# Performance work log

Hardware: AMD Instinct MI355X
Metric: run time of the kernel (lower is better)

Reference implementation:

```python
import jax, jax.numpy as jnp
import numpy as np

N = 50000      # nodes
DEG = 16       # incoming edges per node
E = N * DEG    # edges
F = 256        # nfeat
H = 8          # heads
DH = 32        # nhid // nheads
ALPHA = 0.2    # LeakyReLU negative slope


def setup_inputs() -> dict:
    key = jax.random.key(0)
    ks = jax.random.split(key, 6)
    h = jax.random.normal(ks[0], (N, F), jnp.float32)
    # xavier_uniform-like scale for W (gain 1.414)
    lim_w = 1.414 * np.sqrt(6.0 / (F + DH))
    W = jax.random.uniform(ks[1], (H, F, DH), jnp.float32, -lim_w, lim_w)
    bW = jnp.zeros((H, DH), jnp.float32)
    lim_a = 1.414 * np.sqrt(6.0 / (2 * DH + 1))
    a_src = jax.random.uniform(ks[2], (H, DH), jnp.float32, -lim_a, lim_a)
    a_dst = jax.random.uniform(ks[3], (H, DH), jnp.float32, -lim_a, lim_a)
    a_bias = jnp.zeros((H,), jnp.float32)
    src = jax.random.randint(ks[4], (E,), 0, N, dtype=jnp.int32)
    # every node gets exactly DEG incoming edges (ensures non-empty mailbox)
    dst = jnp.repeat(jnp.arange(N, dtype=jnp.int32), DEG)
    return {"h": h, "W": W, "bW": bW, "a_src": a_src, "a_dst": a_dst,
            "a_bias": a_bias, "src": src, "dst": dst}


def reference(h, W, bW, a_src, a_dst, a_bias, src, dst):
    # per-head projection: Wh[n,h,d]
    Wh = jnp.einsum('nf,hfd->nhd', h, W) + bW
    # decomposed attention linear: a([Wh_src, Wh_dst]) = s1[src] + s2[dst] + b
    s1 = jnp.einsum('nhd,hd->nh', Wh, a_src)   # [N,H]
    s2 = jnp.einsum('nhd,hd->nh', Wh, a_dst)   # [N,H]
    e = jax.nn.leaky_relu(s1[src] + s2[dst] + a_bias, ALPHA)  # [E,H]
    # segment softmax over incoming edges per destination node
    m = jax.ops.segment_max(e, dst, num_segments=N)           # [N,H]
    ex = jnp.exp(e - m[dst])
    denom = jax.ops.segment_sum(ex, dst, num_segments=N)      # [N,H]
    attn = ex / denom[dst]                                    # [E,H]
    # weighted scatter-sum aggregation of source features
    hp = jax.ops.segment_sum(attn[:, :, None] * Wh[src], dst, num_segments=N)  # [N,H,DH]
    # concat heads (matches torch.cat over head outputs)
    return hp.reshape(N, H * DH)
```

## Files before the change

kernel.cpp:

```cpp
#include <hip/hip_runtime.h>

#define NNODES 50000
#define FEAT 256
#define NH 8
#define DHEAD 32
#define DEG 16
#define CDIM 256

typedef __attribute__((ext_vector_type(4))) float floatx4;
typedef __attribute__((ext_vector_type(8))) short shortx8;

__device__ __forceinline__ unsigned short f2bf(float f) {
  union { float f; unsigned u; } v; v.f = f;
  unsigned r = v.u + 0x7fffu + ((v.u >> 16) & 1u);
  return (unsigned short)(r >> 16);
}
__device__ __forceinline__ float bf2f(unsigned short b) {
  union { unsigned u; float f; } v; v.u = ((unsigned)b) << 16;
  return v.f;
}

__global__ __launch_bounds__(256) void convert_wt(
    const float* __restrict__ W, unsigned short* __restrict__ Wt2) {
  int t = blockIdx.x * 256 + threadIdx.x;
#pragma unroll
  for (int p = 0; p < 4; ++p) {
    int idx = t * 4 + p;
    int jj = idx & 7;
    int l = (idx >> 3) & 63;
    int kt = (idx >> 9) & 7;
    int cgrp = idx >> 12;
    int c = cgrp * 16 + (l & 15);
    int f = kt * 32 + ((l >> 4) << 3) + jj;
    Wt2[idx] = f2bf(W[(size_t)(c >> 5) * (FEAT * DHEAD) + (size_t)f * DHEAD + (c & 31)]);
  }
}

__global__ __launch_bounds__(256) void gemm_fused(
    const float* __restrict__ h, const unsigned short* __restrict__ Wt2,
    const float* __restrict__ bW, const float* __restrict__ a_src,
    const float* __restrict__ a_dst, const float* __restrict__ a_bias,
    unsigned short* __restrict__ Whb, float* __restrict__ s1g,
    float* __restrict__ s2g) {
  __shared__ unsigned short As2[8 * 4 * 64 * 8];
  const int tid = threadIdx.x;
  const int w = tid >> 6, lane = tid & 63;
  const int mrow = lane & 15, quad = lane >> 4;
  const int row0 = blockIdx.x * 64;

  {
    int grow = row0 + w * 16 + mrow;
    if (grow > NNODES - 1) grow = NNODES - 1;
    const float* hp = h + (size_t)grow * FEAT + quad * 8;
#pragma unroll
    for (int kt = 0; kt < 8; ++kt) {
      float4 v0 = *(const float4*)(hp + kt * 32);
      float4 v1 = *(const float4*)(hp + kt * 32 + 4);
      shortx8 a8;
      a8[0] = (short)f2bf(v0.x); a8[1] = (short)f2bf(v0.y);
      a8[2] = (short)f2bf(v0.z); a8[3] = (short)f2bf(v0.w);
      a8[4] = (short)f2bf(v1.x); a8[5] = (short)f2bf(v1.y);
      a8[6] = (short)f2bf(v1.z); a8[7] = (short)f2bf(v1.w);
      *(shortx8*)&As2[((kt * 4 + w) * 64 + lane) * 8] = a8;
    }
  }
  __syncthreads();

  floatx4 acc[4][4] = {};
#pragma unroll
  for (int kt = 0; kt < 8; ++kt) {
    shortx8 af[4], bfr[4];
#pragma unroll
    for (int ni = 0; ni < 4; ++ni) {
      int cgrp = w * 4 + ni;
      bfr[ni] = *(const shortx8*)&Wt2[((size_t)(cgrp * 8 + kt) * 64 + lane) * 8];
    }
#pragma unroll
    for (int mi = 0; mi < 4; ++mi)
      af[mi] = *(const shortx8*)&As2[((kt * 4 + mi) * 64 + lane) * 8];
#pragma unroll
    for (int mi = 0; mi < 4; ++mi)
#pragma unroll
      for (int ni = 0; ni < 4; ++ni)
        acc[mi][ni] = __builtin_amdgcn_mfma_f32_16x16x32_bf16(
            af[mi], bfr[ni], acc[mi][ni], 0, 0, 0);
  }

  float aw_s[4], aw_d[4], bias[4];
#pragma unroll
  for (int ni = 0; ni < 4; ++ni) {
    int col = w * 64 + ni * 16 + mrow;
    aw_s[ni] = a_src[col];
    aw_d[ni] = a_dst[col];
    bias[ni] = bW[col];
  }
  float ab0 = a_bias[w * 2], ab1 = a_bias[w * 2 + 1];
#pragma unroll
  for (int mi = 0; mi < 4; ++mi) {
#pragma unroll
    for (int ni = 0; ni < 4; ++ni) {
      int col = w * 64 + ni * 16 + mrow;
#pragma unroll
      for (int r = 0; r < 4; ++r) {
        int row = row0 + mi * 16 + quad * 4 + r;
        float val = acc[mi][ni][r] + bias[ni];
        acc[mi][ni][r] = val;
        if (row < NNODES) Whb[(size_t)row * CDIM + col] = f2bf(val);
      }
    }
#pragma unroll
    for (int r = 0; r < 4; ++r) {
      float s1h0 = acc[mi][0][r] * aw_s[0] + acc[mi][1][r] * aw_s[1];
      float s1h1 = acc[mi][2][r] * aw_s[2] + acc[mi][3][r] * aw_s[3];
      float s2h0 = acc[mi][0][r] * aw_d[0] + acc[mi][1][r] * aw_d[1];
      float s2h1 = acc[mi][2][r] * aw_d[2] + acc[mi][3][r] * aw_d[3];
#pragma unroll
      for (int off = 1; off < 16; off <<= 1) {
        s1h0 += __shfl_xor(s1h0, off, 64);
        s1h1 += __shfl_xor(s1h1, off, 64);
        s2h0 += __shfl_xor(s2h0, off, 64);
        s2h1 += __shfl_xor(s2h1, off, 64);
      }
      if (mrow == 0) {
        int row = row0 + mi * 16 + quad * 4 + r;
        if (row < NNODES) {
          float2 s1v; s1v.x = s1h0; s1v.y = s1h1;
          float2 s2v; s2v.x = s2h0 + ab0; s2v.y = s2h1 + ab1;
          *(float2*)&s1g[(size_t)row * NH + w * 2] = s1v;
          *(float2*)&s2g[(size_t)row * NH + w * 2] = s2v;
        }
      }
    }
  }
}

__global__ __launch_bounds__(256) void aggregate(
    const unsigned short* __restrict__ Whb, const float* __restrict__ s1g,
    const float* __restrict__ s2g, const int* __restrict__ src,
    float* __restrict__ out) {
  __shared__ int srcs_s[4][DEG];
  __shared__ float sc_s[4][DEG * NH];
  int wave = threadIdx.x >> 6, lane = threadIdx.x & 63;
  int n = blockIdx.x * 4 + wave;
  if (lane < DEG) srcs_s[wave][lane] = src[(size_t)n * DEG + lane];
  __syncthreads();

  ushort4 vrows[DEG];
#pragma unroll
  for (int e = 0; e < DEG; ++e)
    vrows[e] = *(const ushort4*)&Whb[(size_t)srcs_s[wave][e] * CDIM + lane * 4];

  int hh7 = lane & 7;
  float s2v = s2g[(size_t)n * NH + hh7];
#pragma unroll
  for (int p = 0; p < 2; ++p) {
    int i = lane + p * 64;
    int e = i >> 3;
    int s = srcs_s[wave][e];
    float sc = s1g[(size_t)s * NH + hh7] + s2v;
    sc_s[wave][i] = sc > 0.f ? sc : 0.2f * sc;
  }
  __syncthreads();
  if (lane < 8) {
    float m = -1e30f;
#pragma unroll
    for (int e = 0; e < DEG; ++e) m = fmaxf(m, sc_s[wave][e * 8 + lane]);
    float sum = 0.f;
#pragma unroll
    for (int e = 0; e < DEG; ++e) {
      float ex = __expf(sc_s[wave][e * 8 + lane] - m);
      sc_s[wave][e * 8 + lane] = ex;
      sum += ex;
    }
    float inv = 1.f / sum;
#pragma unroll
    for (int e = 0; e < DEG; ++e) sc_s[wave][e * 8 + lane] *= inv;
  }
  __syncthreads();

  int hh = lane >> 3;
  floatx4 acc = {0.f, 0.f, 0.f, 0.f};
#pragma unroll
  for (int e = 0; e < DEG; ++e) {
    float wgt = sc_s[wave][e * 8 + hh];
    ushort4 v = vrows[e];
    acc.x += wgt * bf2f(v.x);
    acc.y += wgt * bf2f(v.y);
    acc.z += wgt * bf2f(v.z);
    acc.w += wgt * bf2f(v.w);
  }
  __builtin_nontemporal_store(acc, (floatx4*)&out[(size_t)n * CDIM + lane * 4]);
}

extern "C" void kernel_launch(void* const* d_in, const int* in_sizes, int n_in,
                              void* d_out, int out_size, void* d_ws, size_t ws_size,
                              hipStream_t stream) {
  const float* h = (const float*)d_in[0];
  const float* W = (const float*)d_in[1];
  const float* bW = (const float*)d_in[2];
  const float* a_src = (const float*)d_in[3];
  const float* a_dst = (const float*)d_in[4];
  const float* a_bias = (const float*)d_in[5];
  const int* src = (const int*)d_in[6];
  float* out = (float*)d_out;

  unsigned short* Whb = (unsigned short*)d_ws;
  unsigned short* Wt2 = Whb + (size_t)NNODES * CDIM;
  float* s1g = (float*)(Wt2 + CDIM * FEAT);
  float* s2g = s1g + (size_t)NNODES * NH;

  convert_wt<<<64, 256, 0, stream>>>(W, Wt2);
  gemm_fused<<<(NNODES + 63) / 64, 256, 0, stream>>>(h, Wt2, bW, a_src, a_dst,
                                                     a_bias, Whb, s1g, s2g);
  aggregate<<<NNODES / 4, 256, 0, stream>>>(Whb, s1g, s2g, src, out);
}
```

Measured before the change: 198.3 us.

## Rewrite aggregate kernel with wave shuffles instead of shared memory and barriers

Replaces the shared-memory staging of source indices and attention scores, and the three block barriers, with wave-level shuffles. The segment softmax is now computed cooperatively by all 64 lanes through xor-shuffle reductions, instead of only 8 lanes looping serially over 16 edges. Feature gathers use 16-byte loads, with each half-wave covering half of the edges; the two partial sums are combined by a cross-half shuffle before a select-and-store. This is meant to cut barrier and LDS latency and serial softmax work, at the cost of extra shuffle instructions and higher register pressure.

```diff
diff --git a/kernel.cpp b/kernel.cpp
--- a/kernel.cpp
+++ b/kernel.cpp
@@ -9,6 +9,7 @@
 
 typedef __attribute__((ext_vector_type(4))) float floatx4;
 typedef __attribute__((ext_vector_type(8))) short shortx8;
+typedef __attribute__((ext_vector_type(8))) unsigned short ushortx8;
 
 __device__ __forceinline__ unsigned short f2bf(float f) {
   union { float f; unsigned u; } v; v.f = f;
@@ -138,58 +139,70 @@
     const unsigned short* __restrict__ Whb, const float* __restrict__ s1g,
     const float* __restrict__ s2g, const int* __restrict__ src,
     float* __restrict__ out) {
-  __shared__ int srcs_s[4][DEG];
-  __shared__ float sc_s[4][DEG * NH];
-  int wave = threadIdx.x >> 6, lane = threadIdx.x & 63;
-  int n = blockIdx.x * 4 + wave;
-  if (lane < DEG) srcs_s[wave][lane] = src[(size_t)n * DEG + lane];
-  __syncthreads();
-
-  ushort4 vrows[DEG];
-#pragma unroll
-  for (int e = 0; e < DEG; ++e)
-    vrows[e] = *(const ushort4*)&Whb[(size_t)srcs_s[wave][e] * CDIM + lane * 4];
-
-  int hh7 = lane & 7;
-  float s2v = s2g[(size_t)n * NH + hh7];
-#pragma unroll
-  for (int p = 0; p < 2; ++p) {
-    int i = lane + p * 64;
-    int e = i >> 3;
-    int s = srcs_s[wave][e];
-    float sc = s1g[(size_t)s * NH + hh7] + s2v;
-    sc_s[wave][i] = sc > 0.f ? sc : 0.2f * sc;
-  }
-  __syncthreads();
-  if (lane < 8) {
-    float m = -1e30f;
-#pragma unroll
-    for (int e = 0; e < DEG; ++e) m = fmaxf(m, sc_s[wave][e * 8 + lane]);
-    float sum = 0.f;
-#pragma unroll
-    for (int e = 0; e < DEG; ++e) {
-      float ex = __expf(sc_s[wave][e * 8 + lane] - m);
-      sc_s[wave][e * 8 + lane] = ex;
-      sum += ex;
-    }
-    float inv = 1.f / sum;
-#pragma unroll
-    for (int e = 0; e < DEG; ++e) sc_s[wave][e * 8 + lane] *= inv;
-  }
-  __syncthreads();
-
-  int hh = lane >> 3;
-  floatx4 acc = {0.f, 0.f, 0.f, 0.f};
-#pragma unroll
-  for (int e = 0; e < DEG; ++e) {
-    float wgt = sc_s[wave][e * 8 + hh];
-    ushort4 v = vrows[e];
-    acc.x += wgt * bf2f(v.x);
-    acc.y += wgt * bf2f(v.y);
-    acc.z += wgt * bf2f(v.z);
-    acc.w += wgt * bf2f(v.w);
-  }
-  __builtin_nontemporal_store(acc, (floatx4*)&out[(size_t)n * CDIM + lane * 4]);
+  const int lane = threadIdx.x & 63;
+  const int n = blockIdx.x * 4 + (threadIdx.x >> 6);
+  const int half = lane >> 5;
+  const int l32 = lane & 31;
+  const int hsc = lane & 7;
+  const int hacc = l32 >> 2;
+
+  int s0 = src[(size_t)n * DEG + (lane & 15)];
+  float s2v = s2g[(size_t)n * NH + hsc];
+
+  int se0 = __shfl(s0, lane >> 3);
+  int se1 = __shfl(s0, (lane >> 3) + 8);
+  float s1a = s1g[(size_t)se0 * NH + hsc];
+  float s1b = s1g[(size_t)se1 * NH + hsc];
+
+  int rsrc[8];
+#pragma unroll
+  for (int t = 0; t < 8; ++t) rsrc[t] = __shfl(s0, 2 * t + half);
+  ushortx8 vrow[8];
+#pragma unroll
+  for (int t = 0; t < 8; ++t)
+    vrow[t] = *(const ushortx8*)&Whb[(size_t)rsrc[t] * CDIM + l32 * 8];
+
+  float sc0 = s1a + s2v; sc0 = sc0 > 0.f ? sc0 : 0.2f * sc0;
+  float sc1 = s1b + s2v; sc1 = sc1 > 0.f ? sc1 : 0.2f * sc1;
+  float m = fmaxf(sc0, sc1);
+  m = fmaxf(m, __shfl_xor(m, 8));
+  m = fmaxf(m, __shfl_xor(m, 16));
+  m = fmaxf(m, __shfl_xor(m, 32));
+  float ex0 = __expf(sc0 - m), ex1 = __expf(sc1 - m);
+  float sum = ex0 + ex1;
+  sum += __shfl_xor(sum, 8);
+  sum += __shfl_xor(sum, 16);
+  sum += __shfl_xor(sum, 32);
+  float inv = 1.f / sum;
+  float w0 = ex0 * inv;
+  float w1 = ex1 * inv;
+
+  float wgt[8];
+#pragma unroll
+  for (int t = 0; t < 4; ++t) {
+    int sl = ((2 * t + half) << 3) | hacc;
+    wgt[t] = __shfl(w0, sl);
+    wgt[t + 4] = __shfl(w1, sl);
+  }
+
+  float acc[8] = {0.f, 0.f, 0.f, 0.f, 0.f, 0.f, 0.f, 0.f};
+#pragma unroll
+  for (int t = 0; t < 8; ++t) {
+    ushortx8 v = vrow[t];
+    float w = wgt[t];
+#pragma unroll
+    for (int j = 0; j < 8; ++j) acc[j] += w * bf2f(v[j]);
+  }
+
+#pragma unroll
+  for (int j = 0; j < 8; ++j) acc[j] += __shfl_xor(acc[j], 32);
+  floatx4 o;
+  o.x = half ? acc[4] : acc[0];
+  o.y = half ? acc[5] : acc[1];
+  o.z = half ? acc[6] : acc[2];
+  o.w = half ? acc[7] : acc[3];
+  __builtin_nontemporal_store(
+      o, (floatx4*)&out[(size_t)n * CDIM + l32 * 8 + half * 4]);
 }
 
 extern "C" void kernel_launch(void* const* d_in, const int* in_sizes, int n_in,
```

Result: no change. 198.8 us (+0.2%).

## Store Wh head-major and aggregate per head with wave-shuffle softmax

Applied to the files above, without the earlier changes.

The GEMM now writes the bf16 projected features in a head-major layout ([H][N][32]) instead of node-major. The aggregation kernel is reorganized so each block handles one head for 16 nodes, with 16 lanes per node doing the edge softmax via shuffles instead of shared memory and syncthreads. Each gathered row is now a 64-byte head slice, where the old layout read all 256 features at once. This gives smaller, head-local working sets and removes the barriers, at the cost of 8x more blocks, repeated src/s2 loads per head, and scattered 32-byte partial-row output stores.

```diff
diff --git a/kernel.cpp b/kernel.cpp
--- a/kernel.cpp
+++ b/kernel.cpp
@@ -9,6 +9,7 @@
 
 typedef __attribute__((ext_vector_type(4))) float floatx4;
 typedef __attribute__((ext_vector_type(8))) short shortx8;
+typedef __attribute__((ext_vector_type(8))) unsigned short ushortx8;
 
 __device__ __forceinline__ unsigned short f2bf(float f) {
   union { float f; unsigned u; } v; v.f = f;
@@ -100,12 +101,13 @@
 #pragma unroll
     for (int ni = 0; ni < 4; ++ni) {
       int col = w * 64 + ni * 16 + mrow;
+      const size_t hbase = (size_t)(col >> 5) * ((size_t)NNODES * 32) + (col & 31);
 #pragma unroll
       for (int r = 0; r < 4; ++r) {
         int row = row0 + mi * 16 + quad * 4 + r;
         float val = acc[mi][ni][r] + bias[ni];
         acc[mi][ni][r] = val;
-        if (row < NNODES) Whb[(size_t)row * CDIM + col] = f2bf(val);
+        if (row < NNODES) Whb[hbase + (size_t)row * 32] = f2bf(val);
       }
     }
 #pragma unroll
@@ -138,58 +140,61 @@
     const unsigned short* __restrict__ Whb, const float* __restrict__ s1g,
     const float* __restrict__ s2g, const int* __restrict__ src,
     float* __restrict__ out) {
-  __shared__ int srcs_s[4][DEG];
-  __shared__ float sc_s[4][DEG * NH];
-  int wave = threadIdx.x >> 6, lane = threadIdx.x & 63;
-  int n = blockIdx.x * 4 + wave;
-  if (lane < DEG) srcs_s[wave][lane] = src[(size_t)n * DEG + lane];
-  __syncthreads();
-
-  ushort4 vrows[DEG];
-#pragma unroll
-  for (int e = 0; e < DEG; ++e)
-    vrows[e] = *(const ushort4*)&Whb[(size_t)srcs_s[wave][e] * CDIM + lane * 4];
-
-  int hh7 = lane & 7;
-  float s2v = s2g[(size_t)n * NH + hh7];
-#pragma unroll
-  for (int p = 0; p < 2; ++p) {
-    int i = lane + p * 64;
-    int e = i >> 3;
-    int s = srcs_s[wave][e];
-    float sc = s1g[(size_t)s * NH + hh7] + s2v;
-    sc_s[wave][i] = sc > 0.f ? sc : 0.2f * sc;
-  }
-  __syncthreads();
-  if (lane < 8) {
-    float m = -1e30f;
-#pragma unroll
-    for (int e = 0; e < DEG; ++e) m = fmaxf(m, sc_s[wave][e * 8 + lane]);
-    float sum = 0.f;
-#pragma unroll
-    for (int e = 0; e < DEG; ++e) {
-      float ex = __expf(sc_s[wave][e * 8 + lane] - m);
-      sc_s[wave][e * 8 + lane] = ex;
-      sum += ex;
-    }
-    float inv = 1.f / sum;
-#pragma unroll
-    for (int e = 0; e < DEG; ++e) sc_s[wave][e * 8 + lane] *= inv;
-  }
-  __syncthreads();
-
-  int hh = lane >> 3;
-  floatx4 acc = {0.f, 0.f, 0.f, 0.f};
-#pragma unroll
-  for (int e = 0; e < DEG; ++e) {
-    float wgt = sc_s[wave][e * 8 + hh];
-    ushort4 v = vrows[e];
-    acc.x += wgt * bf2f(v.x);
-    acc.y += wgt * bf2f(v.y);
-    acc.z += wgt * bf2f(v.z);
-    acc.w += wgt * bf2f(v.w);
-  }
-  __builtin_nontemporal_store(acc, (floatx4*)&out[(size_t)n * CDIM + lane * 4]);
+  const int lane = threadIdx.x & 63;
+  const int wv = threadIdx.x >> 6;
+  const int b = blockIdx.x;
+  const int hh = b & 7;
+  const int n = (b >> 3) * 16 + wv * 4 + (lane >> 4);
+  const int e16 = lane & 15;
+
+  int s0 = src[(size_t)n * DEG + e16];
+
+  const int c = lane & 3, e4 = (lane >> 2) & 3;
+  const unsigned short* Wh = Whb + (size_t)hh * ((size_t)NNODES * 32);
+  int rs[4];
+#pragma unroll
+  for (int k = 0; k < 4; ++k) rs[k] = __shfl(s0, (lane & 48) | (e4 + 4 * k));
+  ushortx8 v[4];
+#pragma unroll
+  for (int k = 0; k < 4; ++k)
+    v[k] = *(const ushortx8*)&Wh[(size_t)rs[k] * 32 + c * 8];
+
+  float sc = s1g[(size_t)s0 * NH + hh] + s2g[(size_t)n * NH + hh];
+  sc = sc > 0.f ? sc : 0.2f * sc;
+  float m = sc;
+  m = fmaxf(m, __shfl_xor(m, 1));
+  m = fmaxf(m, __shfl_xor(m, 2));
+  m = fmaxf(m, __shfl_xor(m, 4));
+  m = fmaxf(m, __shfl_xor(m, 8));
+  float ex = __expf(sc - m);
+  float sum = ex;
+  sum += __shfl_xor(sum, 1);
+  sum += __shfl_xor(sum, 2);
+  sum += __shfl_xor(sum, 4);
+  sum += __shfl_xor(sum, 8);
+  float w = ex * (1.f / sum);
+
+  float acc[8] = {0.f, 0.f, 0.f, 0.f, 0.f, 0.f, 0.f, 0.f};
+#pragma unroll
+  for (int k = 0; k < 4; ++k) {
+    float wk = __shfl(w, (lane & 48) | (e4 + 4 * k));
+    ushortx8 vk = v[k];
+#pragma unroll
+    for (int j = 0; j < 8; ++j) acc[j] += wk * bf2f(vk[j]);
+  }
+#pragma unroll
+  for (int j = 0; j < 8; ++j) {
+    acc[j] += __shfl_xor(acc[j], 4);
+    acc[j] += __shfl_xor(acc[j], 8);
+  }
+  if ((lane & 12) == 0) {
+    float* op = &out[(size_t)n * CDIM + hh * 32 + c * 8];
+    floatx4 o0, o1;
+    o0.x = acc[0]; o0.y = acc[1]; o0.z = acc[2]; o0.w = acc[3];
+    o1.x = acc[4]; o1.y = acc[5]; o1.z = acc[6]; o1.w = acc[7];
+    __builtin_nontemporal_store(o0, (floatx4*)op);
+    __builtin_nontemporal_store(o1, (floatx4*)(op + 4));
+  }
 }
 
 extern "C" void kernel_launch(void* const* d_in, const int* in_sizes, int n_in,
@@ -212,5 +217,5 @@
   convert_wt<<<64, 256, 0, stream>>>(W, Wt2);
   gemm_fused<<<(NNODES + 63) / 64, 256, 0, stream>>>(h, Wt2, bW, a_src, a_dst,
                                                      a_bias, Whb, s1g, s2g);
-  aggregate<<<NNODES / 4, 256, 0, stream>>>(Whb, s1g, s2g, src, out);
-}
+  aggregate<<<25000, 256, 0, stream>>>(Whb, s1g, s2g, src, out);
+}
```

Measured after the change: 204.1 us. 1.03x slower.
